# Optimization experiments

Hardware: AMD Instinct MI355X
Metric: run time of the kernel (lower is better)

The kernel has to match this reference:

```python
import jax, jax.numpy as jnp
import numpy as np

N_NODES = 100000

def gcn_conv(x, edge_index, W, b, n_nodes):
    # GCNConv: out = D^{-1/2} (A + I) D^{-1/2} X W + b  (self-loops added)
    src, dst = edge_index[0], edge_index[1]
    loops = jnp.arange(n_nodes, dtype=edge_index.dtype)
    src = jnp.concatenate([src, loops])
    dst = jnp.concatenate([dst, loops])
    deg = jax.ops.segment_sum(jnp.ones_like(dst, dtype=x.dtype), dst, num_segments=n_nodes)
    dinv = jnp.where(deg > 0, jax.lax.rsqrt(deg), 0.0)
    norm = dinv[src] * dinv[dst]  # [E+N]
    h = x @ W  # transform first (small d), then gather/scatter
    msgs = h[src] * norm[:, None]
    out = jax.ops.segment_sum(msgs, dst, num_segments=n_nodes)
    return out + b


def setup_inputs() -> dict:
    key = jax.random.key(0)
    k1, k2, k3, k4, k5, k6 = jax.random.split(key, 6)
    x = jax.random.normal(k1, (N_NODES, 3), dtype=jnp.float32)
    edge_index = jax.random.randint(k2, (2, 2400000), 0, N_NODES, dtype=jnp.int64)
    # Glorot-style init for GCNConv linear weights; zero bias matches PyG default
    W1 = jax.random.normal(k3, (3, 16), dtype=jnp.float32) * (1.0 / np.sqrt(3))
    b1 = jnp.zeros((16,), dtype=jnp.float32)
    W2 = jax.random.normal(k4, (16, 32), dtype=jnp.float32) * (1.0 / np.sqrt(16))
    b2 = jnp.zeros((32,), dtype=jnp.float32)
    return {"x": x, "edge_index": edge_index, "W1": W1, "b1": b1, "W2": W2, "b2": b2}


def reference(x, edge_index, W1, b1, W2, b2):
    n = x.shape[0]
    h = gcn_conv(x, edge_index, W1, b1, n)
    h = jax.nn.relu(h)
    h = gcn_conv(h, edge_index, W2, b2, n)
    # batch is all zeros in the original forward -> single-graph mean pool
    return jnp.mean(h, axis=0, keepdims=True)  # [1, 32]
```

## Files before the change

kernel.cpp:

```cpp
#include <hip/hip_runtime.h>

typedef unsigned int uint;
typedef unsigned long long ull;
typedef unsigned char uchar;


#define MAXB  256
#define CAP   16384u
#define BINB  512
#define CHUNK 4096
#define AFS   2048.0f
#define AFB   16384
#define AFM   0x1FFFFFu
#define PADN  131072

__global__ void __launch_bounds__(BINB)
bin2_kernel(const int* __restrict__ srcI, const int* __restrict__ dstI,
            uint* __restrict__ curDg, uint* __restrict__ curSg,
            uint* __restrict__ bufD, uint* __restrict__ bufS, int E) {
    __shared__ uint cntD[MAXB], scanD[MAXB], deltaD[MAXB];
    __shared__ uint cntS[MAXB], scanS[MAXB], deltaS[MAXB];
    __shared__ uint stageD[CHUNK];
    __shared__ uint stageS[CHUNK];
    __shared__ uchar stBD[CHUNK];
    __shared__ uchar stBS[CHUNK];
    const int tid = threadIdx.x;
    const int e0 = blockIdx.x * CHUNK;
    const int nE = min(CHUNK, E - e0);
    const int my0 = tid * 8;
    const int myc = max(0, min(8, nE - my0));
    if (tid < MAXB) cntD[tid] = 0u; else cntS[tid - MAXB] = 0u;

    uint d8[8], s8[8], rD[8], rS[8];
    if (myc == 8) {
        int4 ka = ((const int4*)(dstI + e0))[tid * 2];
        int4 kb = ((const int4*)(dstI + e0))[tid * 2 + 1];
        int4 oa = ((const int4*)(srcI + e0))[tid * 2];
        int4 ob = ((const int4*)(srcI + e0))[tid * 2 + 1];
        d8[0] = ka.x; d8[1] = ka.y; d8[2] = ka.z; d8[3] = ka.w;
        d8[4] = kb.x; d8[5] = kb.y; d8[6] = kb.z; d8[7] = kb.w;
        s8[0] = oa.x; s8[1] = oa.y; s8[2] = oa.z; s8[3] = oa.w;
        s8[4] = ob.x; s8[5] = ob.y; s8[6] = ob.z; s8[7] = ob.w;
    } else {
        for (int r = 0; r < myc; ++r) {
            d8[r] = (uint)dstI[e0 + my0 + r];
            s8[r] = (uint)srcI[e0 + my0 + r];
        }
    }
    __syncthreads();
    for (int r = 0; r < myc; ++r) {
        rD[r] = atomicAdd(&cntD[d8[r] >> 9], 1u);
        rS[r] = atomicAdd(&cntS[s8[r] >> 9], 1u);
    }
    __syncthreads();
    const int half = tid >> 8;
    const int li = tid & 255;
    uint* cn = half ? cntS : cntD;
    uint* sc = half ? scanS : scanD;
    sc[li] = cn[li];
    __syncthreads();
    for (int d = 1; d < MAXB; d <<= 1) {
        uint t = (li >= d) ? sc[li - d] : 0u;
        __syncthreads();
        sc[li] += t;
        __syncthreads();
    }
    {
        uint* cur = half ? curSg : curDg;
        uint* dl = half ? deltaS : deltaD;
        uint gbase = (uint)li * CAP + (cn[li] ? atomicAdd(&cur[li * 16], cn[li]) : 0u);
        dl[li] = gbase - (sc[li] - cn[li]);
    }
    __syncthreads();
    for (int r = 0; r < myc; ++r) {
        uint bD = d8[r] >> 9;
        uint pD = (scanD[bD] - cntD[bD]) + rD[r];
        stageD[pD] = ((d8[r] & 511u) << 17) | s8[r];
        stBD[pD] = (uchar)bD;
        uint bS = s8[r] >> 9;
        uint pS = (scanS[bS] - cntS[bS]) + rS[r];
        stageS[pS] = ((s8[r] & 511u) << 17) | d8[r];
        stBS[pS] = (uchar)bS;
    }
    __syncthreads();
#pragma unroll
    for (int r = 0; r < 8; ++r) {
        int i = r * BINB + tid;
        if (i < nE) {
            uint b = stBD[i];
            uint gp = deltaD[b] + (uint)i;
            if (gp < (b + 1u) * CAP) bufD[gp] = stageD[i];
            uint b2 = stBS[i];
            uint gp2 = deltaS[b2] + (uint)i;
            if (gp2 < (b2 + 1u) * CAP) bufS[gp2] = stageS[i];
        }
    }
}

__global__ void __launch_bounds__(1024)
degnode_kernel(const uint* __restrict__ buf, const uint* __restrict__ curD,
               const float* __restrict__ x, uint* __restrict__ degg,
               float* __restrict__ dinv, float4* __restrict__ xd4, int n) {
    __shared__ uint dg[512];
    const int tid = threadIdx.x;
    const int b = blockIdx.x;
    const uint base = (uint)b * CAP;
    const uint c = min(curD[b * 16], CAP);
    if (tid < 512) dg[tid] = 0u;
    __syncthreads();
    for (uint i0 = (uint)tid * 8u; i0 < c; i0 += 8192u) {
        uint cnt8 = min(8u, c - i0);
        uint en[8];
        if (cnt8 == 8u) {
            uint4 a = ((const uint4*)(buf + base + i0))[0];
            uint4 bb = ((const uint4*)(buf + base + i0))[1];
            en[0] = a.x; en[1] = a.y; en[2] = a.z; en[3] = a.w;
            en[4] = bb.x; en[5] = bb.y; en[6] = bb.z; en[7] = bb.w;
        } else {
            for (uint r = 0; r < cnt8; ++r) en[r] = buf[base + i0 + r];
        }
        for (uint r = 0; r < cnt8; ++r) atomicAdd(&dg[en[r] >> 17], 1u);
    }
    __syncthreads();
    if (tid < 512) {
        int node = (b << 9) + tid;
        if (node < n) {
            uint d = dg[tid];
            degg[node] = d;
            float di = rsqrtf((float)(d + 1u));
            dinv[node] = di;
            xd4[node] = make_float4(x[3 * node] * di, x[3 * node + 1] * di,
                                    x[3 * node + 2] * di, di);
        }
    }
}

__global__ void __launch_bounds__(1024)
aggqT_kernel(const uint* __restrict__ bufD, const uint* __restrict__ curD,
             const uint* __restrict__ bufS, const uint* __restrict__ curS,
             const uint* __restrict__ degg, const float* __restrict__ dinv,
             const float4* __restrict__ xd4, const float* __restrict__ W1,
             const float* __restrict__ b1, const float* __restrict__ W2,
             const float* __restrict__ b2, float* __restrict__ T,
             uint* __restrict__ doneCtr, float* __restrict__ out, int n) {
    __shared__ ull acc[512];
    __shared__ float gl[512];
    __shared__ float taccs[16];
    __shared__ float tval[16];
    __shared__ int lastB;
    const int tid = threadIdx.x;
    const int b = blockIdx.x;
    const uint base = (uint)b * CAP;
    const uint cD = min(curD[b * 16], CAP);
    const uint cS = min(curS[b * 16], CAP);
    if (tid < 512) { acc[tid] = 0ull; gl[tid] = 0.0f; }
    if (tid < 16) taccs[tid] = 0.0f;
    __syncthreads();
    const int sweep = tid >> 9;
    const uint ht = (uint)(tid & 511);
    if (sweep == 0) {
        for (uint i0 = ht * 8u; i0 < cS; i0 += 4096u) {
            uint cnt8 = min(8u, cS - i0);
            uint en[8];
            if (cnt8 == 8u) {
                uint4 a = ((const uint4*)(bufS + base + i0))[0];
                uint4 bb = ((const uint4*)(bufS + base + i0))[1];
                en[0] = a.x; en[1] = a.y; en[2] = a.z; en[3] = a.w;
                en[4] = bb.x; en[5] = bb.y; en[6] = bb.z; en[7] = bb.w;
            } else {
                for (uint r = 0; r < cnt8; ++r) en[r] = bufS[base + i0 + r];
                for (uint r = cnt8; r < 8u; ++r) en[r] = en[0];
            }
            float dv[8];
#pragma unroll
            for (int r = 0; r < 8; ++r) dv[r] = dinv[en[r] & 0x1FFFFu];
#pragma unroll
            for (uint r = 0; r < 8u; ++r)
                if (r < cnt8) atomicAdd(&gl[en[r] >> 17], dv[r]);
        }
    } else {
        for (uint i0 = ht * 8u; i0 < cD; i0 += 4096u) {
            uint cnt8 = min(8u, cD - i0);
            uint en[8];
            if (cnt8 == 8u) {
                uint4 a = ((const uint4*)(bufD + base + i0))[0];
                uint4 bb = ((const uint4*)(bufD + base + i0))[1];
                en[0] = a.x; en[1] = a.y; en[2] = a.z; en[3] = a.w;
                en[4] = bb.x; en[5] = bb.y; en[6] = bb.z; en[7] = bb.w;
            } else {
                for (uint r = 0; r < cnt8; ++r) en[r] = bufD[base + i0 + r];
                for (uint r = cnt8; r < 8u; ++r) en[r] = en[0];
            }
            float4 gv[8];
#pragma unroll
            for (int r = 0; r < 8; ++r) gv[r] = xd4[en[r] & 0x1FFFFu];
#pragma unroll
            for (uint r = 0; r < 8u; ++r) {
                if (r < cnt8) {
                    uint dl = en[r] >> 17;
                    ull f0 = (ull)(uint)((int)rintf(gv[r].x * AFS) + AFB);
                    ull f1 = (ull)(uint)((int)rintf(gv[r].y * AFS) + AFB);
                    ull f2 = (ull)(uint)((int)rintf(gv[r].z * AFS) + AFB);
                    atomicAdd(&acc[dl], f0 | (f1 << 21) | (f2 << 42));
                }
            }
        }
    }
    __syncthreads();
    float sq[16];
#pragma unroll
    for (int k = 0; k < 16; ++k) sq[k] = 0.0f;
    if (tid < 512) {
        int node = (b << 9) + tid;
        if (node < n) {
            ull v = acc[tid];
            int ub = (int)(degg[node] * (uint)AFB);
            float4 sv = xd4[node];
            float di = sv.w;
            const float isc = 1.0f / AFS;
            float av = (float)((int)(uint)(v & AFM) - ub) * isc + sv.x;
            float bv = (float)((int)(uint)((v >> 21) & AFM) - ub) * isc + sv.y;
            float cv = (float)((int)(uint)((v >> 42) & AFM) - ub) * isc + sv.z;
            float w = gl[tid] + di;
#pragma unroll
            for (int k = 0; k < 16; ++k) {
                float h = di * (av * W1[k] + bv * W1[16 + k] + cv * W1[32 + k]) + b1[k];
                h = fmaxf(h, 0.0f);
                sq[k] = w * (di * h);
            }
        }
    }
#pragma unroll
    for (int k = 0; k < 16; ++k) {
        float v2 = sq[k];
        for (int off = 32; off > 0; off >>= 1) v2 += __shfl_down(v2, off, 64);
        if ((tid & 63) == 0) atomicAdd(&taccs[k], v2);
    }
    __syncthreads();
    if (tid < 16 && taccs[tid] != 0.0f) atomicAdd(&T[tid], taccs[tid]);
    __syncthreads();
    if (tid == 0) {
        __threadfence();
        uint t = atomicAdd(doneCtr, 1u);
        lastB = (t == (uint)(gridDim.x - 1)) ? 1 : 0;
    }
    __syncthreads();
    if (lastB) {
        if (tid < 16) tval[tid] = atomicAdd(&T[tid], 0.0f);
        __syncthreads();
        if (tid < 32) {
            float s2 = 0.0f;
#pragma unroll
            for (int k = 0; k < 16; ++k) s2 += tval[k] * W2[k * 32 + tid];
            out[tid] = b2[tid] + (1.0f / (float)n) * s2;
        }
    }
}

extern "C" void kernel_launch(void* const* d_in, const int* in_sizes, int n_in,
                              void* d_out, int out_size, void* d_ws, size_t ws_size,
                              hipStream_t stream) {
    const float* x   = (const float*)d_in[0];
    const int*   ei  = (const int*)d_in[1];
    const float* W1  = (const float*)d_in[2];
    const float* b1  = (const float*)d_in[3];
    const float* W2  = (const float*)d_in[4];
    const float* b2  = (const float*)d_in[5];
    float* out = (float*)d_out;

    const int n = in_sizes[0] / 3;
    const int E = in_sizes[1] / 2;
    const int* src = ei;
    const int* dst = ei + E;

    char* p = (char*)d_ws;
    float* T    = (float*)p;    p += 64;
    uint*  done = (uint*)p;     p += 64;
    uint*  curD = (uint*)p;     p += MAXB * 16 * 4;
    uint*  curS = (uint*)p;     p += MAXB * 16 * 4;
    size_t zbytes = (size_t)(p - (char*)d_ws);
    uint*  degg  = (uint*)p;    p += (size_t)n * 4;
    float* dinv  = (float*)p;   p += (size_t)n * 4;
    uint*  bufD  = (uint*)p;    p += (size_t)MAXB * CAP * 4;
    uint*  bufS  = (uint*)p;    p += (size_t)MAXB * CAP * 4;
    p = (char*)(((size_t)p + 31) & ~(size_t)31);
    float4* xd4  = (float4*)p;  p += (size_t)PADN * 16;

    const int nb = (n + 511) >> 9;

    hipMemsetAsync(d_ws, 0, zbytes, stream);
    bin2_kernel<<<(E + CHUNK - 1) / CHUNK, BINB, 0, stream>>>(src, dst, curD, curS, bufD, bufS, E);
    degnode_kernel<<<nb, 1024, 0, stream>>>(bufD, curD, x, degg, dinv, xd4, n);
    aggqT_kernel<<<nb, 1024, 0, stream>>>(bufD, curD, bufS, curS, degg, dinv, xd4,
                                          W1, b1, W2, b2, T, done, out, n);
}
```

Measured before the change: 135.4 us.

## Drop source-binned edge buffer; scatter source weights via global atomics

The edge binning now builds only the destination-binned buffer, which halves the binning scatter traffic and shared staging. The per-source sum of dinv[dst] that the source-binned sweep used to compute is now gathered with global float atomicAdd inside the destination sweep. Node features are pre-quantized into packed 64-bit fixed-point words in degnode, so the aggregation loads 8 bytes per edge with no conversion. Layer-1 outputs are stored as bf16 and reduced in a separate kernel, which adds a launch, a global atomic per edge and bf16 rounding error.

Measured after the change: 240.0 us. +77.2%, slower.

```diff
diff --git a/kernel.cpp b/kernel.cpp
--- a/kernel.cpp
+++ b/kernel.cpp
@@ -15,23 +15,19 @@
 #define PADN  131072
 
 __global__ void __launch_bounds__(BINB)
-bin2_kernel(const int* __restrict__ srcI, const int* __restrict__ dstI,
-            uint* __restrict__ curDg, uint* __restrict__ curSg,
-            uint* __restrict__ bufD, uint* __restrict__ bufS, int E) {
-    __shared__ uint cntD[MAXB], scanD[MAXB], deltaD[MAXB];
-    __shared__ uint cntS[MAXB], scanS[MAXB], deltaS[MAXB];
-    __shared__ uint stageD[CHUNK];
-    __shared__ uint stageS[CHUNK];
-    __shared__ uchar stBD[CHUNK];
-    __shared__ uchar stBS[CHUNK];
+bin1_kernel(const int* __restrict__ srcI, const int* __restrict__ dstI,
+            uint* __restrict__ curDg, uint* __restrict__ bufD, int E) {
+    __shared__ uint cnt[MAXB], scanb[MAXB], delta[MAXB];
+    __shared__ uint stage[CHUNK];
+    __shared__ uchar stB[CHUNK];
     const int tid = threadIdx.x;
     const int e0 = blockIdx.x * CHUNK;
     const int nE = min(CHUNK, E - e0);
     const int my0 = tid * 8;
     const int myc = max(0, min(8, nE - my0));
-    if (tid < MAXB) cntD[tid] = 0u; else cntS[tid - MAXB] = 0u;
-
-    uint d8[8], s8[8], rD[8], rS[8];
+    if (tid < MAXB) cnt[tid] = 0u;
+
+    uint d8[8], s8[8], r8[8];
     if (myc == 8) {
         int4 ka = ((const int4*)(dstI + e0))[tid * 2];
         int4 kb = ((const int4*)(dstI + e0))[tid * 2 + 1];
@@ -48,51 +44,35 @@
         }
     }
     __syncthreads();
+    for (int r = 0; r < myc; ++r) r8[r] = atomicAdd(&cnt[d8[r] >> 9], 1u);
+    __syncthreads();
+    if (tid < MAXB) scanb[tid] = cnt[tid];
+    __syncthreads();
+    for (int d = 1; d < MAXB; d <<= 1) {
+        uint t = (tid < MAXB && tid >= d) ? scanb[tid - d] : 0u;
+        __syncthreads();
+        if (tid < MAXB) scanb[tid] += t;
+        __syncthreads();
+    }
+    if (tid < MAXB) {
+        uint gbase = (uint)tid * CAP + (cnt[tid] ? atomicAdd(&curDg[tid * 16], cnt[tid]) : 0u);
+        delta[tid] = gbase - (scanb[tid] - cnt[tid]);
+    }
+    __syncthreads();
     for (int r = 0; r < myc; ++r) {
-        rD[r] = atomicAdd(&cntD[d8[r] >> 9], 1u);
-        rS[r] = atomicAdd(&cntS[s8[r] >> 9], 1u);
-    }
-    __syncthreads();
-    const int half = tid >> 8;
-    const int li = tid & 255;
-    uint* cn = half ? cntS : cntD;
-    uint* sc = half ? scanS : scanD;
-    sc[li] = cn[li];
-    __syncthreads();
-    for (int d = 1; d < MAXB; d <<= 1) {
-        uint t = (li >= d) ? sc[li - d] : 0u;
-        __syncthreads();
-        sc[li] += t;
-        __syncthreads();
-    }
-    {
-        uint* cur = half ? curSg : curDg;
-        uint* dl = half ? deltaS : deltaD;
-        uint gbase = (uint)li * CAP + (cn[li] ? atomicAdd(&cur[li * 16], cn[li]) : 0u);
-        dl[li] = gbase - (sc[li] - cn[li]);
-    }
-    __syncthreads();
-    for (int r = 0; r < myc; ++r) {
-        uint bD = d8[r] >> 9;
-        uint pD = (scanD[bD] - cntD[bD]) + rD[r];
-        stageD[pD] = ((d8[r] & 511u) << 17) | s8[r];
-        stBD[pD] = (uchar)bD;
-        uint bS = s8[r] >> 9;
-        uint pS = (scanS[bS] - cntS[bS]) + rS[r];
-        stageS[pS] = ((s8[r] & 511u) << 17) | d8[r];
-        stBS[pS] = (uchar)bS;
+        uint b = d8[r] >> 9;
+        uint pD = (scanb[b] - cnt[b]) + r8[r];
+        stage[pD] = ((d8[r] & 511u) << 17) | s8[r];
+        stB[pD] = (uchar)b;
     }
     __syncthreads();
 #pragma unroll
     for (int r = 0; r < 8; ++r) {
         int i = r * BINB + tid;
         if (i < nE) {
-            uint b = stBD[i];
-            uint gp = deltaD[b] + (uint)i;
-            if (gp < (b + 1u) * CAP) bufD[gp] = stageD[i];
-            uint b2 = stBS[i];
-            uint gp2 = deltaS[b2] + (uint)i;
-            if (gp2 < (b2 + 1u) * CAP) bufS[gp2] = stageS[i];
+            uint b = stB[i];
+            uint gp = delta[b] + (uint)i;
+            if (gp < (b + 1u) * CAP) bufD[gp] = stage[i];
         }
     }
 }
@@ -100,7 +80,7 @@
 __global__ void __launch_bounds__(1024)
 degnode_kernel(const uint* __restrict__ buf, const uint* __restrict__ curD,
                const float* __restrict__ x, uint* __restrict__ degg,
-               float* __restrict__ dinv, float4* __restrict__ xd4, int n) {
+               float* __restrict__ dinv, ull* __restrict__ pxd, int n) {
     __shared__ uint dg[512];
     const int tid = threadIdx.x;
     const int b = blockIdx.x;
@@ -129,105 +109,117 @@
             degg[node] = d;
             float di = rsqrtf((float)(d + 1u));
             dinv[node] = di;
-            xd4[node] = make_float4(x[3 * node] * di, x[3 * node + 1] * di,
-                                    x[3 * node + 2] * di, di);
+            float tx = x[3 * node] * di;
+            float ty = x[3 * node + 1] * di;
+            float tz = x[3 * node + 2] * di;
+            ull f0 = (ull)(uint)((int)rintf(tx * AFS) + AFB);
+            ull f1 = (ull)(uint)((int)rintf(ty * AFS) + AFB);
+            ull f2 = (ull)(uint)((int)rintf(tz * AFS) + AFB);
+            pxd[node] = f0 | (f1 << 21) | (f2 << 42);
         }
     }
 }
 
 __global__ void __launch_bounds__(1024)
-aggqT_kernel(const uint* __restrict__ bufD, const uint* __restrict__ curD,
-             const uint* __restrict__ bufS, const uint* __restrict__ curS,
-             const uint* __restrict__ degg, const float* __restrict__ dinv,
-             const float4* __restrict__ xd4, const float* __restrict__ W1,
-             const float* __restrict__ b1, const float* __restrict__ W2,
-             const float* __restrict__ b2, float* __restrict__ T,
-             uint* __restrict__ doneCtr, float* __restrict__ out, int n) {
+aggq_kernel(const uint* __restrict__ bufD, const uint* __restrict__ curD,
+            const uint* __restrict__ degg, const float* __restrict__ dinv,
+            const ull* __restrict__ pxd, const float* __restrict__ x,
+            const float* __restrict__ W1, const float* __restrict__ b1,
+            float* __restrict__ g, uint4* __restrict__ qb, int n) {
     __shared__ ull acc[512];
-    __shared__ float gl[512];
-    __shared__ float taccs[16];
-    __shared__ float tval[16];
-    __shared__ int lastB;
+    __shared__ float dt[512];
     const int tid = threadIdx.x;
     const int b = blockIdx.x;
     const uint base = (uint)b * CAP;
-    const uint cD = min(curD[b * 16], CAP);
-    const uint cS = min(curS[b * 16], CAP);
-    if (tid < 512) { acc[tid] = 0ull; gl[tid] = 0.0f; }
-    if (tid < 16) taccs[tid] = 0.0f;
-    __syncthreads();
-    const int sweep = tid >> 9;
-    const uint ht = (uint)(tid & 511);
-    if (sweep == 0) {
-        for (uint i0 = ht * 8u; i0 < cS; i0 += 4096u) {
-            uint cnt8 = min(8u, cS - i0);
-            uint en[8];
-            if (cnt8 == 8u) {
-                uint4 a = ((const uint4*)(bufS + base + i0))[0];
-                uint4 bb = ((const uint4*)(bufS + base + i0))[1];
-                en[0] = a.x; en[1] = a.y; en[2] = a.z; en[3] = a.w;
-                en[4] = bb.x; en[5] = bb.y; en[6] = bb.z; en[7] = bb.w;
-            } else {
-                for (uint r = 0; r < cnt8; ++r) en[r] = bufS[base + i0 + r];
-                for (uint r = cnt8; r < 8u; ++r) en[r] = en[0];
+    const uint c = min(curD[b * 16], CAP);
+    if (tid < 512) {
+        acc[tid] = 0ull;
+        int node = (b << 9) + tid;
+        dt[tid] = (node < n) ? dinv[node] : 0.0f;
+    }
+    __syncthreads();
+    for (uint i0 = (uint)tid * 8u; i0 < c; i0 += 8192u) {
+        uint cnt8 = min(8u, c - i0);
+        uint en[8];
+        if (cnt8 == 8u) {
+            uint4 a = ((const uint4*)(bufD + base + i0))[0];
+            uint4 bb = ((const uint4*)(bufD + base + i0))[1];
+            en[0] = a.x; en[1] = a.y; en[2] = a.z; en[3] = a.w;
+            en[4] = bb.x; en[5] = bb.y; en[6] = bb.z; en[7] = bb.w;
+        } else {
+            for (uint r = 0; r < cnt8; ++r) en[r] = bufD[base + i0 + r];
+            for (uint r = cnt8; r < 8u; ++r) en[r] = en[0];
+        }
+        ull gv[8];
+#pragma unroll
+        for (int r = 0; r < 8; ++r) gv[r] = pxd[en[r] & 0x1FFFFu];
+#pragma unroll
+        for (uint r = 0; r < 8u; ++r) {
+            if (r < cnt8) {
+                uint dl = en[r] >> 17;
+                atomicAdd(&acc[dl], gv[r]);
+                atomicAdd(&g[en[r] & 0x1FFFFu], dt[dl]);
             }
-            float dv[8];
-#pragma unroll
-            for (int r = 0; r < 8; ++r) dv[r] = dinv[en[r] & 0x1FFFFu];
-#pragma unroll
-            for (uint r = 0; r < 8u; ++r)
-                if (r < cnt8) atomicAdd(&gl[en[r] >> 17], dv[r]);
-        }
-    } else {
-        for (uint i0 = ht * 8u; i0 < cD; i0 += 4096u) {
-            uint cnt8 = min(8u, cD - i0);
-            uint en[8];
-            if (cnt8 == 8u) {
-                uint4 a = ((const uint4*)(bufD + base + i0))[0];
-                uint4 bb = ((const uint4*)(bufD + base + i0))[1];
-                en[0] = a.x; en[1] = a.y; en[2] = a.z; en[3] = a.w;
-                en[4] = bb.x; en[5] = bb.y; en[6] = bb.z; en[7] = bb.w;
-            } else {
-                for (uint r = 0; r < cnt8; ++r) en[r] = bufD[base + i0 + r];
-                for (uint r = cnt8; r < 8u; ++r) en[r] = en[0];
-            }
-            float4 gv[8];
-#pragma unroll
-            for (int r = 0; r < 8; ++r) gv[r] = xd4[en[r] & 0x1FFFFu];
-#pragma unroll
-            for (uint r = 0; r < 8u; ++r) {
-                if (r < cnt8) {
-                    uint dl = en[r] >> 17;
-                    ull f0 = (ull)(uint)((int)rintf(gv[r].x * AFS) + AFB);
-                    ull f1 = (ull)(uint)((int)rintf(gv[r].y * AFS) + AFB);
-                    ull f2 = (ull)(uint)((int)rintf(gv[r].z * AFS) + AFB);
-                    atomicAdd(&acc[dl], f0 | (f1 << 21) | (f2 << 42));
-                }
-            }
-        }
-    }
-    __syncthreads();
-    float sq[16];
-#pragma unroll
-    for (int k = 0; k < 16; ++k) sq[k] = 0.0f;
+        }
+    }
+    __syncthreads();
     if (tid < 512) {
         int node = (b << 9) + tid;
         if (node < n) {
             ull v = acc[tid];
             int ub = (int)(degg[node] * (uint)AFB);
-            float4 sv = xd4[node];
-            float di = sv.w;
+            float di = dt[tid];
             const float isc = 1.0f / AFS;
-            float av = (float)((int)(uint)(v & AFM) - ub) * isc + sv.x;
-            float bv = (float)((int)(uint)((v >> 21) & AFM) - ub) * isc + sv.y;
-            float cv = (float)((int)(uint)((v >> 42) & AFM) - ub) * isc + sv.z;
-            float w = gl[tid] + di;
+            float av = (float)((int)(uint)(v & AFM) - ub) * isc + x[3 * node] * di;
+            float bv = (float)((int)(uint)((v >> 21) & AFM) - ub) * isc + x[3 * node + 1] * di;
+            float cv = (float)((int)(uint)((v >> 42) & AFM) - ub) * isc + x[3 * node + 2] * di;
+            float qv[16];
 #pragma unroll
             for (int k = 0; k < 16; ++k) {
                 float h = di * (av * W1[k] + bv * W1[16 + k] + cv * W1[32 + k]) + b1[k];
                 h = fmaxf(h, 0.0f);
-                sq[k] = w * (di * h);
+                qv[k] = di * h;
             }
+            uint pk[8];
+#pragma unroll
+            for (int k = 0; k < 8; ++k) {
+                uint l = __float_as_uint(qv[2 * k]);
+                l = (l + 0x7FFFu + ((l >> 16) & 1u)) >> 16;
+                uint h2 = __float_as_uint(qv[2 * k + 1]);
+                h2 = ((h2 + 0x7FFFu + ((h2 >> 16) & 1u)) & 0xFFFF0000u);
+                pk[k] = l | h2;
+            }
+            qb[2 * (size_t)node]     = make_uint4(pk[0], pk[1], pk[2], pk[3]);
+            qb[2 * (size_t)node + 1] = make_uint4(pk[4], pk[5], pk[6], pk[7]);
+        }
+    }
+}
+
+__global__ void __launch_bounds__(256)
+Tq_kernel(const uint4* __restrict__ qb, const float* __restrict__ g,
+          const float* __restrict__ dinv, const float* __restrict__ W2,
+          const float* __restrict__ b2, float* __restrict__ T,
+          uint* __restrict__ doneCtr, float* __restrict__ out,
+          int n, float invN) {
+    __shared__ float taccs[16];
+    __shared__ float tval[16];
+    __shared__ int lastB;
+    const int tid = threadIdx.x;
+    const int i = blockIdx.x * 256 + tid;
+    if (tid < 16) taccs[tid] = 0.0f;
+    __syncthreads();
+    float sq[16];
+#pragma unroll
+    for (int k = 0; k < 16; ++k) sq[k] = 0.0f;
+    if (i < n) {
+        uint4 qa = qb[2 * (size_t)i];
+        uint4 qc = qb[2 * (size_t)i + 1];
+        float w = g[i] + dinv[i];
+        uint pw[8] = {qa.x, qa.y, qa.z, qa.w, qc.x, qc.y, qc.z, qc.w};
+#pragma unroll
+        for (int k = 0; k < 8; ++k) {
+            sq[2 * k]     = w * __uint_as_float(pw[k] << 16);
+            sq[2 * k + 1] = w * __uint_as_float(pw[k] & 0xFFFF0000u);
         }
     }
 #pragma unroll
@@ -252,7 +244,7 @@
             float s2 = 0.0f;
 #pragma unroll
             for (int k = 0; k < 16; ++k) s2 += tval[k] * W2[k * 32 + tid];
-            out[tid] = b2[tid] + (1.0f / (float)n) * s2;
+            out[tid] = b2[tid] + invN * s2;
         }
     }
 }
@@ -277,20 +269,21 @@
     float* T    = (float*)p;    p += 64;
     uint*  done = (uint*)p;     p += 64;
     uint*  curD = (uint*)p;     p += MAXB * 16 * 4;
-    uint*  curS = (uint*)p;     p += MAXB * 16 * 4;
+    float* g    = (float*)p;    p += (size_t)n * 4;
     size_t zbytes = (size_t)(p - (char*)d_ws);
     uint*  degg  = (uint*)p;    p += (size_t)n * 4;
     float* dinv  = (float*)p;   p += (size_t)n * 4;
     uint*  bufD  = (uint*)p;    p += (size_t)MAXB * CAP * 4;
-    uint*  bufS  = (uint*)p;    p += (size_t)MAXB * CAP * 4;
     p = (char*)(((size_t)p + 31) & ~(size_t)31);
-    float4* xd4  = (float4*)p;  p += (size_t)PADN * 16;
+    ull*   pxd   = (ull*)p;     p += (size_t)PADN * 8;
+    uint4* qb    = (uint4*)p;   p += (size_t)n * 32;
 
     const int nb = (n + 511) >> 9;
+    const int nbq = (n + 255) >> 8;
 
     hipMemsetAsync(d_ws, 0, zbytes, stream);
-    bin2_kernel<<<(E + CHUNK - 1) / CHUNK, BINB, 0, stream>>>(src, dst, curD, curS, bufD, bufS, E);
-    degnode_kernel<<<nb, 1024, 0, stream>>>(bufD, curD, x, degg, dinv, xd4, n);
-    aggqT_kernel<<<nb, 1024, 0, stream>>>(bufD, curD, bufS, curS, degg, dinv, xd4,
-                                          W1, b1, W2, b2, T, done, out, n);
-}
+    bin1_kernel<<<(E + CHUNK - 1) / CHUNK, BINB, 0, stream>>>(src, dst, curD, bufD, E);
+    degnode_kernel<<<nb, 1024, 0, stream>>>(bufD, curD, x, degg, dinv, pxd, n);
+    aggq_kernel<<<nb, 1024, 0, stream>>>(bufD, curD, degg, dinv, pxd, x, W1, b1, g, qb, n);
+    Tq_kernel<<<nbq, 256, 0, stream>>>(qb, g, dinv, W2, b2, T, done, out, n, 1.0f / (float)n);
+}
```
